# Kernel optimization log

Measured on AMD Instinct MI355X. Metric: run time of the kernel, lower is better.

Reference implementation:

```python
import jax, jax.numpy as jnp
import numpy as np

B = 128          # batch
T = 196          # total_patches per view (2 views -> 2*T tokens)
ENC = 1024       # encoder_embed_dim
DEC = 512        # decoder_embed_dim
V = 98           # num unmasked (visible) tokens per sample
M = 2 * T - V    # num masked tokens (294)


def setup_inputs() -> dict:
    key = jax.random.key(0)
    kx, kperm, kw, kmt, kpos, kview = jax.random.split(key, 6)
    x = jax.random.normal(kx, (B, V, ENC), jnp.float32)
    # masked_ids: unique ids per row in [0, 2T) — built from permutations
    perms = jax.vmap(jax.random.permutation, in_axes=(0, None))(
        jax.random.split(kperm, B), 2 * T)
    masked_ids = perms[:, :M].astype(jnp.int64)
    W = jax.random.normal(kw, (DEC, ENC), jnp.float32) * 0.02
    b = jnp.zeros((DEC,), jnp.float32)
    mask_token = jax.random.normal(kmt, (1, 1, DEC), jnp.float32)
    pos_embed = jax.random.normal(kpos, (1, 2 * T, DEC), jnp.float32)
    view_embed = jax.random.normal(kview, (2, DEC), jnp.float32)
    return {"x": x, "masked_ids": masked_ids, "W": W, "b": b,
            "mask_token": mask_token, "pos_embed": pos_embed,
            "view_embed": view_embed}


def reference(x, masked_ids, W, b, mask_token, pos_embed, view_embed):
    Bn = x.shape[0]
    # Linear: enc -> dec
    xp = jnp.einsum('bve,de->bvd', x, W) + b          # (B, V, DEC)
    # visible ids = sorted complement of masked_ids (vectorized, no batch loop)
    rows = jnp.arange(Bn)[:, None]
    vis_mask = jnp.ones((Bn, 2 * T), bool).at[rows, masked_ids].set(False)
    # stable argsort puts True(visible, ~mask=False) positions first, in order
    visible_ids = jnp.argsort(~vis_mask, axis=1)[:, :V]  # (B, V)
    # scatter projected visible tokens into mask-token placeholders
    base = jnp.broadcast_to(mask_token, (Bn, 2 * T, DEC))
    view = base.at[rows, visible_ids].set(xp)          # (B, 2T, DEC)
    # per-view embedding: first T tokens -> view 0, last T -> view 1
    ve = jnp.concatenate([
        jnp.broadcast_to(view_embed[0], (T, DEC)),
        jnp.broadcast_to(view_embed[1], (T, DEC))], axis=0)  # (2T, DEC)
    return view + pos_embed + ve[None, :, :]
```

## Files before the change

kernel.cpp:

```cpp
#include <hip/hip_runtime.h>

#define BATCH 128
#define VIS   98
#define TOK   196
#define TOK2  392
#define ENC   1024
#define DEC   512
#define MSK   294

#define NWB 256

#define NGEMM 784
#define NFILL 1568

typedef __bf16 bf16x8 __attribute__((ext_vector_type(8)));
typedef float  f32x4  __attribute__((ext_vector_type(4)));

__device__ __forceinline__ unsigned short f2bf(float f) {
    union { float f; unsigned u; } c; c.f = f;
    unsigned u = c.u;
    return (unsigned short)((u + 0x7fffu + ((u >> 16) & 1u)) >> 16);
}

__device__ __forceinline__ void g2lds16(const void* gptr, void* lptr) {
    __builtin_amdgcn_global_load_lds(
        (const __attribute__((address_space(1))) void*)gptr,
        (__attribute__((address_space(3))) void*)lptr, 16, 0, 0);
}

__global__ __launch_bounds__(512) void setup(const float* __restrict__ W,
                                             const int* __restrict__ mids,
                                             unsigned short* __restrict__ wbm,
                                             int* __restrict__ visids,
                                             unsigned char* __restrict__ flags) {
    int bid = blockIdx.x, tid = threadIdx.x;
    if (bid < NWB) {
        int i = bid * 512 + tid;
        float4 f = ((const float4*)W)[i];
        ushort4 o;
        o.x = f2bf(f.x); o.y = f2bf(f.y); o.z = f2bf(f.z); o.w = f2bf(f.w);
        ((ushort4*)wbm)[i] = o;
        return;
    }
    int b = bid - NWB;
    __shared__ unsigned char lf[TOK2];
    __shared__ int wtot[8];
    if (tid < TOK2) lf[tid] = 1;
    __syncthreads();
    if (tid < MSK) lf[mids[b * MSK + tid]] = 0;
    __syncthreads();
    int flag = (tid < TOK2) ? (int)lf[tid] : 0;
    unsigned long long bal = __ballot(flag != 0);
    int lane = tid & 63, wv = tid >> 6;
    int pre = __popcll(bal & ((1ull << lane) - 1ull));
    if (lane == 0) wtot[wv] = __popcll(bal);
    __syncthreads();
    int off = 0;
    for (int i = 0; i < wv; ++i) off += wtot[i];
    if (flag) visids[b * VIS + off + pre] = tid;
    if (tid < TOK2) flags[b * TOK2 + tid] = lf[tid];
}

__global__ __launch_bounds__(256, 4) void main_fused(
    const float* __restrict__ x,
    const unsigned short* __restrict__ wb,
    const float* __restrict__ bias,
    const float* __restrict__ mask_token,
    const float* __restrict__ pos,
    const float* __restrict__ ve,
    const int* __restrict__ vis,
    const unsigned char* __restrict__ flags,
    float* __restrict__ out) {
    __shared__ float Asf[64 * 64];
    __shared__ unsigned short Bs[128 * 64];
    __shared__ int rowdst[64];
    __shared__ int rowt[64];

    int bid = blockIdx.x;
    int tid = threadIdx.x;

    if (bid >= NGEMM) {
        int fb = bid - NGEMM;
        float4 m = ((const float4*)mask_token)[tid & 127];
        int g0 = fb * 4096 + tid;
        #pragma unroll 4
        for (int i = 0; i < 16; ++i) {
            int g = g0 + i * 256;
            int tok = g >> 7;
            int d4  = g & 127;
            if (flags[tok]) continue;
            int t = tok % TOK2;
            float4 p = ((const float4*)(pos + (size_t)t * DEC))[d4];
            float4 v = ((const float4*)(ve + (t >= TOK ? DEC : 0)))[d4];
            float4 r;
            r.x = m.x + p.x + v.x;
            r.y = m.y + p.y + v.y;
            r.z = m.z + p.z + v.z;
            r.w = m.w + p.w + v.w;
            ((float4*)out)[g] = r;
        }
        return;
    }

    int lane = tid & 63, w = tid >> 6;
    int l16 = lane & 15, q = lane >> 4;
    int wm = w & 1, wn = w >> 1;
    int m0 = (bid >> 2) * 64, n0 = (bid & 3) * 128;

    if (tid < 64) {
        int gr = m0 + tid;
        int t = vis[gr];
        rowt[tid] = t;
        rowdst[tid] = (gr / VIS) * TOK2 + t;
    }

    int arow = tid >> 4;
    int cA = (tid & 15) ^ arow;
    const float* gA = x + (size_t)(m0 + arow) * ENC + cA * 4;
    char* ldsA = (char*)Asf + tid * 16;
    int cB = (tid & 7) ^ ((tid >> 3) & 7);
    const unsigned short* gB = wb + (size_t)(n0 + (tid >> 3)) * ENC + cB * 8;
    char* ldsB = (char*)Bs + tid * 16;

    f32x4 acc[2][4];
    #pragma unroll
    for (int i = 0; i < 2; ++i)
        #pragma unroll
        for (int j = 0; j < 4; ++j)
            acc[i][j] = (f32x4){0.f, 0.f, 0.f, 0.f};

    for (int k0 = 0; k0 < ENC; k0 += 64) {
        __syncthreads();
        #pragma unroll
        for (int t = 0; t < 4; ++t)
            g2lds16(gB + (size_t)t * 32 * ENC + k0, ldsB + t * 4096);
        #pragma unroll
        for (int t = 0; t < 4; ++t)
            g2lds16(gA + (size_t)t * 16 * ENC + k0, ldsA + t * 4096);
        __syncthreads();

        #pragma unroll
        for (int u = 0; u < 2; ++u) {
            int slotB = ((u * 4 + q) ^ (l16 & 7)) * 16;
            int c0 = u * 8 + q * 2;
            bf16x8 bfrag[4], afrag[2];
            #pragma unroll
            for (int j = 0; j < 4; ++j)
                bfrag[j] = *(const bf16x8*)((const char*)Bs + (wn * 64 + j * 16 + l16) * 128 + slotB);
            #pragma unroll
            for (int i = 0; i < 2; ++i) {
                const char* rowbase = (const char*)Asf + (wm * 32 + i * 16 + l16) * 256;
                f32x4 lo = *(const f32x4*)(rowbase + ((c0 ^ l16) * 16));
                f32x4 hi = *(const f32x4*)(rowbase + (((c0 + 1) ^ l16) * 16));
                bf16x8 af;
                af[0] = (__bf16)lo[0]; af[1] = (__bf16)lo[1];
                af[2] = (__bf16)lo[2]; af[3] = (__bf16)lo[3];
                af[4] = (__bf16)hi[0]; af[5] = (__bf16)hi[1];
                af[6] = (__bf16)hi[2]; af[7] = (__bf16)hi[3];
                afrag[i] = af;
            }
            #pragma unroll
            for (int i = 0; i < 2; ++i)
                #pragma unroll
                for (int j = 0; j < 4; ++j)
                    acc[i][j] = __builtin_amdgcn_mfma_f32_16x16x32_bf16(afrag[i], bfrag[j], acc[i][j], 0, 0, 0);
        }
    }

    #pragma unroll
    for (int j = 0; j < 4; ++j) {
        int gcol = n0 + wn * 64 + j * 16 + l16;
        float bc = bias[gcol];
        float v0 = ve[gcol];
        float v1 = ve[DEC + gcol];
        #pragma unroll
        for (int i = 0; i < 2; ++i) {
            #pragma unroll
            for (int r = 0; r < 4; ++r) {
                int rl = wm * 32 + i * 16 + q * 4 + r;
                int t = rowt[rl];
                float val = acc[i][j][r] + bc + pos[(size_t)t * DEC + gcol]
                          + (t >= TOK ? v1 : v0);
                out[(size_t)rowdst[rl] * DEC + gcol] = val;
            }
        }
    }
}

extern "C" void kernel_launch(void* const* d_in, const int* in_sizes, int n_in,
                              void* d_out, int out_size, void* d_ws, size_t ws_size,
                              hipStream_t stream) {
    (void)in_sizes; (void)n_in; (void)out_size; (void)ws_size;
    const float* x    = (const float*)d_in[0];
    const int*   mids = (const int*)d_in[1];
    const float* W    = (const float*)d_in[2];
    const float* bias = (const float*)d_in[3];
    const float* mt   = (const float*)d_in[4];
    const float* pos  = (const float*)d_in[5];
    const float* ve   = (const float*)d_in[6];
    float* out = (float*)d_out;

    unsigned short* wbm = (unsigned short*)d_ws;
    int* visids = (int*)(wbm + (size_t)DEC * ENC);
    unsigned char* flags = (unsigned char*)(visids + BATCH * VIS);

    hipLaunchKernelGGL(setup, dim3(NWB + BATCH), dim3(512), 0, stream,
                       W, mids, wbm, visids, flags);
    hipLaunchKernelGGL(main_fused, dim3(NGEMM + NFILL), dim3(256), 0, stream,
                       x, wbm, bias, mt, pos, ve, visids, flags, out);
}
```

Measured before the change: 193.1 us.

## Double-buffer LDS tiles in GEMM and remap block order for cache reuse

The GEMM's LDS staging is double-buffered: the next K-slice of A and B is fetched with global_load_lds while the current slice feeds MFMA, with explicit vmcnt waits and barriers. Block-to-tile mapping is also reordered so groups of 8 M-tiles share the same N-tile in sequence, which should improve L2 reuse of x and W. LDS use doubles to about 64KB per block, so the occupancy hint is lowered from 4 to 2 blocks per CU. The hand-written vmcnt counts depend on the exact number of outstanding loads.

```diff
diff --git a/kernel.cpp b/kernel.cpp
--- a/kernel.cpp
+++ b/kernel.cpp
@@ -61,7 +61,7 @@
     if (tid < TOK2) flags[b * TOK2 + tid] = lf[tid];
 }
 
-__global__ __launch_bounds__(256, 4) void main_fused(
+__global__ __launch_bounds__(256, 2) void main_fused(
     const float* __restrict__ x,
     const unsigned short* __restrict__ wb,
     const float* __restrict__ bias,
@@ -71,8 +71,8 @@
     const int* __restrict__ vis,
     const unsigned char* __restrict__ flags,
     float* __restrict__ out) {
-    __shared__ float Asf[64 * 64];
-    __shared__ unsigned short Bs[128 * 64];
+    __shared__ float Asf[2][64 * 64];
+    __shared__ unsigned short Bs[2][128 * 64];
     __shared__ int rowdst[64];
     __shared__ int rowt[64];
 
@@ -105,7 +105,11 @@
     int lane = tid & 63, w = tid >> 6;
     int l16 = lane & 15, q = lane >> 4;
     int wm = w & 1, wn = w >> 1;
-    int m0 = (bid >> 2) * 64, n0 = (bid & 3) * 128;
+
+    int mb, nb;
+    if (bid < 768) { mb = (bid & 7) + ((bid >> 5) << 3); nb = (bid >> 3) & 3; }
+    else           { int ii = bid - 768; mb = 192 + (ii & 3); nb = ii >> 2; }
+    int m0 = mb * 64, n0 = nb * 128;
 
     if (tid < 64) {
         int gr = m0 + tid;
@@ -117,10 +121,8 @@
     int arow = tid >> 4;
     int cA = (tid & 15) ^ arow;
     const float* gA = x + (size_t)(m0 + arow) * ENC + cA * 4;
-    char* ldsA = (char*)Asf + tid * 16;
     int cB = (tid & 7) ^ ((tid >> 3) & 7);
     const unsigned short* gB = wb + (size_t)(n0 + (tid >> 3)) * ENC + cB * 8;
-    char* ldsB = (char*)Bs + tid * 16;
 
     f32x4 acc[2][4];
     #pragma unroll
@@ -129,16 +131,40 @@
         for (int j = 0; j < 4; ++j)
             acc[i][j] = (f32x4){0.f, 0.f, 0.f, 0.f};
 
-    for (int k0 = 0; k0 < ENC; k0 += 64) {
-        __syncthreads();
-        #pragma unroll
-        for (int t = 0; t < 4; ++t)
-            g2lds16(gB + (size_t)t * 32 * ENC + k0, ldsB + t * 4096);
-        #pragma unroll
-        for (int t = 0; t < 4; ++t)
-            g2lds16(gA + (size_t)t * 16 * ENC + k0, ldsA + t * 4096);
-        __syncthreads();
-
+    {
+        char* lA = (char*)(&Asf[0][0]) + tid * 16;
+        char* lB = (char*)(&Bs[0][0]) + tid * 16;
+        #pragma unroll
+        for (int tt = 0; tt < 4; ++tt)
+            g2lds16(gB + (size_t)tt * 32 * ENC, lB + tt * 4096);
+        #pragma unroll
+        for (int tt = 0; tt < 4; ++tt)
+            g2lds16(gA + (size_t)tt * 16 * ENC, lA + tt * 4096);
+    }
+    __syncthreads();
+
+    for (int t = 0; t < 16; ++t) {
+        int cur = t & 1;
+        if (t < 15) {
+            int k0 = (t + 1) << 6;
+            char* lA = (char*)(&Asf[cur ^ 1][0]) + tid * 16;
+            char* lB = (char*)(&Bs[cur ^ 1][0]) + tid * 16;
+            #pragma unroll
+            for (int tt = 0; tt < 4; ++tt)
+                g2lds16(gB + (size_t)tt * 32 * ENC + k0, lB + tt * 4096);
+            #pragma unroll
+            for (int tt = 0; tt < 4; ++tt)
+                g2lds16(gA + (size_t)tt * 16 * ENC + k0, lA + tt * 4096);
+            __builtin_amdgcn_sched_barrier(0);
+            asm volatile("s_waitcnt vmcnt(8)" ::: "memory");
+        } else {
+            __builtin_amdgcn_sched_barrier(0);
+            asm volatile("s_waitcnt vmcnt(0)" ::: "memory");
+        }
+        __builtin_amdgcn_s_barrier();
+
+        const char* Ab = (const char*)(&Asf[cur][0]);
+        const char* Bb = (const char*)(&Bs[cur][0]);
         #pragma unroll
         for (int u = 0; u < 2; ++u) {
             int slotB = ((u * 4 + q) ^ (l16 & 7)) * 16;
@@ -146,10 +172,10 @@
             bf16x8 bfrag[4], afrag[2];
             #pragma unroll
             for (int j = 0; j < 4; ++j)
-                bfrag[j] = *(const bf16x8*)((const char*)Bs + (wn * 64 + j * 16 + l16) * 128 + slotB);
+                bfrag[j] = *(const bf16x8*)(Bb + (wn * 64 + j * 16 + l16) * 128 + slotB);
             #pragma unroll
             for (int i = 0; i < 2; ++i) {
-                const char* rowbase = (const char*)Asf + (wm * 32 + i * 16 + l16) * 256;
+                const char* rowbase = Ab + (wm * 32 + i * 16 + l16) * 256;
                 f32x4 lo = *(const f32x4*)(rowbase + ((c0 ^ l16) * 16));
                 f32x4 hi = *(const f32x4*)(rowbase + (((c0 + 1) ^ l16) * 16));
                 bf16x8 af;
@@ -165,6 +191,7 @@
                 for (int j = 0; j < 4; ++j)
                     acc[i][j] = __builtin_amdgcn_mfma_f32_16x16x32_bf16(afrag[i], bfrag[j], acc[i][j], 0, 0, 0);
         }
+        __builtin_amdgcn_s_barrier();
     }
 
     #pragma unroll
```

Measured after the change: 189.0 us. 1.02x faster.
